# Kernel optimization log

Hardware: AMD Instinct MI355X
Metric: run time of the kernel (lower is better)

## Reference

```python
import jax, jax.numpy as jnp
import numpy as np

N_NODES, N_EDGES, N_LAYERS, N_CH, N_GRAPHS = 50000, 1600000, 4, 16, 64
HID = N_CH * 3  # 16x1o -> dim 48

_eps = np.zeros((3, 3, 3), dtype=np.float32)
_eps[0, 1, 2] = _eps[1, 2, 0] = _eps[2, 0, 1] = 1.0
_eps[0, 2, 1] = _eps[2, 1, 0] = _eps[1, 0, 2] = -1.0
EPS = jnp.asarray(_eps)  # Levi-Civita: CG coeffs for 1 (x) 1 -> 1
TP_NORM = 1.0 / np.sqrt(2.0 * N_CH).astype(np.float32)  # CG norm * path fan-in norm


def setup_inputs():
    key = jax.random.key(0)
    ks = jax.random.split(key, 12)
    return {
        "x": jax.random.normal(ks[0], (N_NODES, 3), jnp.float32),
        "edge_index": jax.random.randint(ks[1], (2, N_EDGES), 0, N_NODES, jnp.int32),
        "edge_attr": jax.random.normal(ks[2], (N_EDGES, 5), jnp.float32),
        "batch": jnp.sort(jax.random.randint(ks[3], (N_NODES,), 0, N_GRAPHS, jnp.int32)),
        "embed_w": jax.random.normal(ks[4], (3, HID), jnp.float32) * 0.3,
        "mlp1_w": jax.random.normal(ks[5], (N_LAYERS, 3, 16), jnp.float32) * 0.5,
        "mlp1_b": jnp.zeros((N_LAYERS, 16), jnp.float32),
        "mlp2_w": jax.random.normal(ks[6], (N_LAYERS, 16, HID), jnp.float32) * 0.25,
        "mlp2_b": jnp.zeros((N_LAYERS, HID), jnp.float32),
        "tp_w": jax.random.normal(ks[7], (N_LAYERS, N_CH, N_CH), jnp.float32),
        "lin_w": jax.random.normal(ks[8], (HID, 1), jnp.float32) * 0.1,
        "lin_b": jnp.zeros((1,), jnp.float32),
    }


def reference(x, edge_index, edge_attr, batch, embed_w, mlp1_w, mlp1_b,
              mlp2_w, mlp2_b, tp_w, lin_w, lin_b):
    n = x.shape[0]
    e = edge_attr.shape[0]
    src, dst = edge_index[0], edge_index[1]

    h = x @ embed_w  # [N, 48] node embedding

    r_ij = edge_attr[:, 2:5]                            # [E, 3]
    r2 = jnp.sum(r_ij * r_ij, axis=-1, keepdims=True)   # [E, 1]
    rhat = r_ij / jnp.maximum(jnp.sqrt(r2), 1e-12)
    sh = jnp.sqrt(3.0) * rhat                            # l=1 SH, component norm
    edge_scalar = jnp.concatenate([edge_attr[:, 0:2], r2], axis=-1)  # [E, 3]

    for l in range(N_LAYERS):
        gate = jax.nn.silu(edge_scalar @ mlp1_w[l] + mlp1_b[l]) @ mlp2_w[l] + mlp2_b[l]  # [E,48]
        xj = h[src].reshape(e, N_CH, 3)                  # gather neighbor feats
        # fully-connected tensor product 16x1o (x) 1o -> 16x1o (cross-product CG)
        tp = jnp.einsum('kij,eui,ej,uv->evk', EPS, xj, sh, tp_w[l]) * TP_NORM
        msg = gate * tp.reshape(e, HID)
        dx = jax.ops.segment_sum(msg, dst, num_segments=n)  # scatter-add
        h = h + dx  # residual

    sums = jax.ops.segment_sum(h, batch, num_segments=N_GRAPHS)
    cnt = jax.ops.segment_sum(jnp.ones((n,), h.dtype), batch, num_segments=N_GRAPHS)
    pooled = sums / jnp.maximum(cnt, 1.0)[:, None]       # global mean pool
    return (pooled @ lin_w + lin_b).ravel()              # [B]
```

## Files before the change

### kernel.cpp

```cpp
#include <hip/hip_runtime.h>

#define N_NODES 50000
#define N_EDGES 1600000
#define N_LAYERS 4
#define N_CH 16
#define HID 48
#define N_GRAPHS 64
#define TP_NORM 0.17677669529663687f
#define SQRT3 1.7320508075688772f
#define REB 256
#define MPAD 28
#define NBLK (N_EDGES / REB)
#define NPART ((N_NODES + 255) / 256)

__device__ __forceinline__ unsigned bfpack2(float a, float b) {
    unsigned ua = __float_as_uint(a);
    unsigned ub = __float_as_uint(b);
    ua = (ua + 0x7fffu + ((ua >> 16) & 1u)) >> 16;
    ub = (ub + 0x7fffu + ((ub >> 16) & 1u)) >> 16;
    return ua | (ub << 16);
}
#define BFLO(u) __uint_as_float((u) << 16)
#define BFHI(u) __uint_as_float((u) & 0xffff0000u)

__global__ void k_embed(const float* __restrict__ x, const float* __restrict__ ew,
                        float* __restrict__ h) {
    int t = blockIdx.x * blockDim.x + threadIdx.x;
    if (t >= N_NODES * HID) return;
    int n = t / HID, c = t % HID;
    h[t] = x[n * 3 + 0] * ew[c] + x[n * 3 + 1] * ew[HID + c] + x[n * 3 + 2] * ew[2 * HID + c];
}

__global__ void k_count(const int* __restrict__ ei, int* __restrict__ cnt,
                        int* __restrict__ rank) {
    int e = blockIdx.x * 256 + threadIdx.x;
    rank[e] = atomicAdd(&cnt[ei[N_EDGES + e]], 1);
}

__global__ void k_sred(const int* __restrict__ cnt, int* __restrict__ bsum) {
    __shared__ int red[256];
    int b = blockIdx.x, t = threadIdx.x;
    int idx = b * 256 + t;
    red[t] = (idx < N_NODES) ? cnt[idx] : 0;
    __syncthreads();
    for (int d = 128; d > 0; d >>= 1) {
        if (t < d) red[t] += red[t + d];
        __syncthreads();
    }
    if (t == 0) bsum[b] = red[0];
}

__global__ void k_sscan(const int* __restrict__ bsum, int* __restrict__ bbase) {
    __shared__ int s[256];
    int t = threadIdx.x;
    int v = (t < NPART) ? bsum[t] : 0;
    s[t] = v;
    __syncthreads();
    for (int d = 1; d < 256; d <<= 1) {
        int x = (t >= d) ? s[t - d] : 0;
        __syncthreads();
        s[t] += x;
        __syncthreads();
    }
    if (t < NPART) bbase[t] = s[t] - v;
    if (t == NPART - 1) bbase[NPART] = s[t];
}

__global__ void k_soff(const int* __restrict__ cnt, const int* __restrict__ bbase,
                       int* __restrict__ off) {
    __shared__ int s[256];
    int b = blockIdx.x, t = threadIdx.x;
    int idx = b * 256 + t;
    int v = (idx < N_NODES) ? cnt[idx] : 0;
    s[t] = v;
    __syncthreads();
    for (int d = 1; d < 256; d <<= 1) {
        int x = (t >= d) ? s[t - d] : 0;
        __syncthreads();
        s[t] += x;
        __syncthreads();
    }
    if (idx < N_NODES) off[idx] = bbase[b] + s[t] - v;
    if (idx == 0) off[N_NODES] = bbase[NPART];
}

__global__ void k_rng(const int* __restrict__ off, int* __restrict__ blk) {
    int b = blockIdx.x * blockDim.x + threadIdx.x;
    if (b >= NBLK) return;
    int base = b * REB;
    int lo = 0, hi = N_NODES;
    while (lo < hi) { int mid = (lo + hi + 1) >> 1; if (off[mid] <= base) lo = mid; else hi = mid - 1; }
    blk[2 * b] = lo;
    int last = base + REB - 1;
    int hi2 = N_NODES;
    while (lo < hi2) { int mid = (lo + hi2 + 1) >> 1; if (off[mid] <= last) lo = mid; else hi2 = mid - 1; }
    blk[2 * b + 1] = lo;
}

__global__ void k_build(const int* __restrict__ ei, const float* __restrict__ ea,
                        const int* __restrict__ off, const int* __restrict__ rank,
                        float* __restrict__ es_s) {
    int e = blockIdx.x * 256 + threadIdx.x;
    int d = ei[N_EDGES + e];
    int pos = off[d] + rank[e];
    float a0 = ea[e * 5 + 0], a1 = ea[e * 5 + 1];
    float rx = ea[e * 5 + 2], ry = ea[e * 5 + 3], rz = ea[e * 5 + 4];
    float r2 = rx * rx + ry * ry + rz * rz;
    float inv = rsqrtf(fmaxf(r2, 1e-24f)) * SQRT3;
    float4* o = (float4*)(es_s + (size_t)pos * 8);
    o[0] = make_float4(a0, a1, r2, rx * inv);
    o[1] = make_float4(ry * inv, rz * inv, __int_as_float(ei[e]), 0.f);
}

__global__ void k_h2(const float* __restrict__ hin, const float* __restrict__ tpw,
                     unsigned* __restrict__ h2, float* __restrict__ dx) {
    int t = blockIdx.x * blockDim.x + threadIdx.x;
    if (t >= N_NODES * 24) return;
    int n = t / 24, p = t % 24;
    int c0 = 2 * p, c1 = c0 + 1;
    int v0 = c0 / 3, i0 = c0 % 3;
    int v1 = c1 / 3, i1 = c1 % 3;
    const float* hr = hin + (size_t)n * HID;
    float s0 = 0.f, s1 = 0.f;
#pragma unroll
    for (int u = 0; u < 16; u++) {
        s0 = fmaf(tpw[u * 16 + v0], hr[u * 3 + i0], s0);
        s1 = fmaf(tpw[u * 16 + v1], hr[u * 3 + i1], s1);
    }
    h2[t] = bfpack2(s0, s1);
    *(float2*)(dx + (size_t)n * HID + c0) = make_float2(0.f, 0.f);
}

__global__ void k_h2_add(const float* __restrict__ hin, const float* __restrict__ dxin,
                         const float* __restrict__ tpw,
                         unsigned* __restrict__ h2, float* __restrict__ hout,
                         float* __restrict__ dxout) {
    int t = blockIdx.x * blockDim.x + threadIdx.x;
    if (t >= N_NODES * 24) return;
    int n = t / 24, p = t % 24;
    int c0 = 2 * p, c1 = c0 + 1;
    int v0 = c0 / 3, i0 = c0 % 3;
    int v1 = c1 / 3, i1 = c1 % 3;
    size_t rb = (size_t)n * HID;
    const float* hr = hin + rb;
    const float* dr = dxin + rb;
    float s0 = 0.f, s1 = 0.f;
#pragma unroll
    for (int u = 0; u < 16; u++) {
        float e0 = hr[u * 3 + i0] + dr[u * 3 + i0];
        float e1 = hr[u * 3 + i1] + dr[u * 3 + i1];
        s0 = fmaf(tpw[u * 16 + v0], e0, s0);
        s1 = fmaf(tpw[u * 16 + v1], e1, s1);
    }
    h2[t] = bfpack2(s0, s1);
    float2 hv = *(const float2*)(hr + c0);
    float2 dv = *(const float2*)(dr + c0);
    *(float2*)(hout + rb + c0) = make_float2(hv.x + dv.x, hv.y + dv.y);
    *(float2*)(dxout + rb + c0) = make_float2(0.f, 0.f);
}

__global__ void __launch_bounds__(256) k_fused(
    const float* __restrict__ es_s, const int* __restrict__ off,
    const int* __restrict__ blk,
    const unsigned* __restrict__ h2, float* __restrict__ dx,
    const float* __restrict__ m1w, const float* __restrict__ m1b,
    const float* __restrict__ m2w, const float* __restrict__ m2b)
{
    __shared__ float s_msg[REB][MPAD];

    int t = threadIdx.x;
    int base = blockIdx.x * REB;
    int e2 = base + t;

    const float4* esp = (const float4*)(es_s + (size_t)e2 * 8);
    float4 es0 = esp[0];
    float4 es1 = esp[1];
    int src = __float_as_int(es1.z);
    const uint4* hv = (const uint4*)(h2 + (size_t)src * 24);
    uint4 A0 = hv[0], A1 = hv[1], A2 = hv[2];
    int n0 = blk[2 * blockIdx.x];
    int n1 = blk[2 * blockIdx.x + 1];

    float a0 = es0.x, a1 = es0.y, r2 = es0.z;
    float shx = es0.w, shy = es1.x, shz = es1.y;

    float hid[16];
#pragma unroll
    for (int j = 0; j < 16; j++) {
        float z = fmaf(a0, m1w[j], fmaf(a1, m1w[16 + j], fmaf(r2, m1w[32 + j], m1b[j])));
        hid[j] = z / (1.f + __expf(-z));
    }

    int gid = t / 12;
    int rem = t % 12;
    int q   = rem >> 1;
    int half= rem & 1;

    float xj[24];
#define UNPK8(u, d) { (d)[0]=BFLO((u).x); (d)[1]=BFHI((u).x); (d)[2]=BFLO((u).y); (d)[3]=BFHI((u).y); \
                      (d)[4]=BFLO((u).z); (d)[5]=BFHI((u).z); (d)[6]=BFLO((u).w); (d)[7]=BFHI((u).w); }
    UNPK8(A0, &xj[0]); UNPK8(A1, &xj[8]); UNPK8(A2, &xj[16]);

    float m[24];
#pragma unroll
    for (int qq = 0; qq < 6; qq++) {
        float4 b = *(const float4*)(m2b + qq * 4);
        m[qq * 4 + 0] = b.x; m[qq * 4 + 1] = b.y; m[qq * 4 + 2] = b.z; m[qq * 4 + 3] = b.w;
    }
#pragma unroll
    for (int j = 0; j < 16; j++) {
        float hj = hid[j];
#pragma unroll
        for (int qq = 0; qq < 6; qq++) {
            float4 w4 = *(const float4*)(m2w + j * 48 + qq * 4);
            m[qq * 4 + 0] = fmaf(hj, w4.x, m[qq * 4 + 0]);
            m[qq * 4 + 1] = fmaf(hj, w4.y, m[qq * 4 + 1]);
            m[qq * 4 + 2] = fmaf(hj, w4.z, m[qq * 4 + 2]);
            m[qq * 4 + 3] = fmaf(hj, w4.w, m[qq * 4 + 3]);
        }
    }
#pragma unroll
    for (int v = 0; v < 8; v++) {
        float x0 = xj[v * 3 + 0], x1 = xj[v * 3 + 1], x2 = xj[v * 3 + 2];
        float c0 = x1 * shz - x2 * shy;
        float c1 = x2 * shx - x0 * shz;
        float c2 = x0 * shy - x1 * shx;
        m[v * 3 + 0] *= c0 * TP_NORM;
        m[v * 3 + 1] *= c1 * TP_NORM;
        m[v * 3 + 2] *= c2 * TP_NORM;
    }
    {
        float4* row = (float4*)&s_msg[t][0];
#pragma unroll
        for (int qq = 0; qq < 6; qq++) row[qq] = ((float4*)m)[qq];
    }
    {
        uint4 B0 = hv[3], B1 = hv[4], B2 = hv[5];
        UNPK8(B0, &xj[0]); UNPK8(B1, &xj[8]); UNPK8(B2, &xj[16]);
    }
    __syncthreads();

    if (t < 252) {
        for (int nn = n0 + gid; nn <= n1; nn += 21) {
            int lo = off[nn], hi = off[nn + 1];
            int rlo = (lo > base) ? lo - base : 0;
            int rhi = ((hi < base + REB) ? hi : base + REB) - base;
            if (rlo < rhi) {
                float4 acc = make_float4(0.f, 0.f, 0.f, 0.f);
                for (int r = rlo + half; r < rhi; r += 2) {
                    float4 v = *(const float4*)&s_msg[r][q * 4];
                    acc.x += v.x; acc.y += v.y; acc.z += v.z; acc.w += v.w;
                }
                acc.x += __shfl_xor(acc.x, 1);
                acc.y += __shfl_xor(acc.y, 1);
                acc.z += __shfl_xor(acc.z, 1);
                acc.w += __shfl_xor(acc.w, 1);
                if (half == 0) {
                    float* dp = dx + (size_t)nn * HID + q * 4;
                    if (lo < base || hi > base + REB) {
                        atomicAdd(dp + 0, acc.x); atomicAdd(dp + 1, acc.y);
                        atomicAdd(dp + 2, acc.z); atomicAdd(dp + 3, acc.w);
                    } else {
                        *(float4*)dp = acc;
                    }
                }
            }
        }
    }
    __syncthreads();

#pragma unroll
    for (int qq = 0; qq < 6; qq++) {
        float4 b = *(const float4*)(m2b + 24 + qq * 4);
        m[qq * 4 + 0] = b.x; m[qq * 4 + 1] = b.y; m[qq * 4 + 2] = b.z; m[qq * 4 + 3] = b.w;
    }
#pragma unroll
    for (int j = 0; j < 16; j++) {
        float hj = hid[j];
#pragma unroll
        for (int qq = 0; qq < 6; qq++) {
            float4 w4 = *(const float4*)(m2w + j * 48 + 24 + qq * 4);
            m[qq * 4 + 0] = fmaf(hj, w4.x, m[qq * 4 + 0]);
            m[qq * 4 + 1] = fmaf(hj, w4.y, m[qq * 4 + 1]);
            m[qq * 4 + 2] = fmaf(hj, w4.z, m[qq * 4 + 2]);
            m[qq * 4 + 3] = fmaf(hj, w4.w, m[qq * 4 + 3]);
        }
    }
#pragma unroll
    for (int v = 0; v < 8; v++) {
        float x0 = xj[v * 3 + 0], x1 = xj[v * 3 + 1], x2 = xj[v * 3 + 2];
        float c0 = x1 * shz - x2 * shy;
        float c1 = x2 * shx - x0 * shz;
        float c2 = x0 * shy - x1 * shx;
        m[v * 3 + 0] *= c0 * TP_NORM;
        m[v * 3 + 1] *= c1 * TP_NORM;
        m[v * 3 + 2] *= c2 * TP_NORM;
    }
    {
        float4* row = (float4*)&s_msg[t][0];
#pragma unroll
        for (int qq = 0; qq < 6; qq++) row[qq] = ((float4*)m)[qq];
    }
    __syncthreads();

    if (t < 252) {
        for (int nn = n0 + gid; nn <= n1; nn += 21) {
            int lo = off[nn], hi = off[nn + 1];
            int rlo = (lo > base) ? lo - base : 0;
            int rhi = ((hi < base + REB) ? hi : base + REB) - base;
            if (rlo < rhi) {
                float4 acc = make_float4(0.f, 0.f, 0.f, 0.f);
                for (int r = rlo + half; r < rhi; r += 2) {
                    float4 v = *(const float4*)&s_msg[r][q * 4];
                    acc.x += v.x; acc.y += v.y; acc.z += v.z; acc.w += v.w;
                }
                acc.x += __shfl_xor(acc.x, 1);
                acc.y += __shfl_xor(acc.y, 1);
                acc.z += __shfl_xor(acc.z, 1);
                acc.w += __shfl_xor(acc.w, 1);
                if (half == 0) {
                    float* dp = dx + (size_t)nn * HID + 24 + q * 4;
                    if (lo < base || hi > base + REB) {
                        atomicAdd(dp + 0, acc.x); atomicAdd(dp + 1, acc.y);
                        atomicAdd(dp + 2, acc.z); atomicAdd(dp + 3, acc.w);
                    } else {
                        *(float4*)dp = acc;
                    }
                }
            }
        }
    }
}

__global__ void k_add(float* __restrict__ h, float* __restrict__ dx) {
    int t = blockIdx.x * blockDim.x + threadIdx.x;
    if (t >= N_NODES * HID) return;
    h[t] += dx[t];
    dx[t] = 0.f;
}

__global__ void __launch_bounds__(256) k_pool(
    const float* __restrict__ h, const float* __restrict__ dxin, const int* __restrict__ batch,
    const float* __restrict__ linw, float* __restrict__ gsum, float* __restrict__ gcnt)
{
    __shared__ float ss[N_GRAPHS];
    __shared__ float sc[N_GRAPHS];
    for (int i = threadIdx.x; i < N_GRAPHS; i += 256) { ss[i] = 0.f; sc[i] = 0.f; }
    __syncthreads();
    int n = blockIdx.x * 256 + threadIdx.x;
    if (n < N_NODES) {
        float s = 0.f;
        const float4* hv = (const float4*)(h + (size_t)n * HID);
        const float4* dv = (const float4*)(dxin + (size_t)n * HID);
#pragma unroll
        for (int qq = 0; qq < 12; qq++) {
            float4 v = hv[qq], d = dv[qq];
            s += (v.x + d.x) * linw[qq * 4 + 0] + (v.y + d.y) * linw[qq * 4 + 1]
               + (v.z + d.z) * linw[qq * 4 + 2] + (v.w + d.w) * linw[qq * 4 + 3];
        }
        int b = batch[n];
        atomicAdd(&ss[b], s);
        atomicAdd(&sc[b], 1.f);
    }
    __syncthreads();
    for (int i = threadIdx.x; i < N_GRAPHS; i += 256) {
        if (sc[i] != 0.f) {
            atomicAdd(&gsum[i], ss[i]);
            atomicAdd(&gcnt[i], sc[i]);
        }
    }
}

__global__ void k_final(const float* __restrict__ gsum, const float* __restrict__ gcnt,
                        const float* __restrict__ linb, float* __restrict__ out) {
    int g = threadIdx.x;
    if (g < N_GRAPHS) out[g] = gsum[g] / fmaxf(gcnt[g], 1.f) + linb[0];
}

__global__ void __launch_bounds__(256) k_edge_atomic(
    const int* __restrict__ ei, const float* __restrict__ ea,
    const float* __restrict__ h, float* __restrict__ dx,
    const float* __restrict__ m1w, const float* __restrict__ m1b,
    const float* __restrict__ m2w, const float* __restrict__ m2b,
    const float* __restrict__ tpw)
{
    __shared__ float s_m1w[48];
    __shared__ float s_m1b[16];
    __shared__ float s_m2w[768];
    __shared__ float s_m2b[48];
    __shared__ float s_tpw[256];
    for (int i = threadIdx.x; i < 48;  i += 256) s_m1w[i] = m1w[i];
    for (int i = threadIdx.x; i < 16;  i += 256) s_m1b[i] = m1b[i];
    for (int i = threadIdx.x; i < 768; i += 256) s_m2w[i] = m2w[i];
    for (int i = threadIdx.x; i < 48;  i += 256) s_m2b[i] = m2b[i];
    for (int i = threadIdx.x; i < 256; i += 256) s_tpw[i] = tpw[i];
    __syncthreads();
    int e = blockIdx.x * 256 + threadIdx.x;
    int src = ei[e];
    int dst = ei[N_EDGES + e];
    float a0 = ea[e * 5 + 0], a1 = ea[e * 5 + 1];
    float rx = ea[e * 5 + 2], ry = ea[e * 5 + 3], rz = ea[e * 5 + 4];
    float r2 = rx * rx + ry * ry + rz * rz;
    float inv = rsqrtf(fmaxf(r2, 1e-24f));
    float shx = SQRT3 * rx * inv, shy = SQRT3 * ry * inv, shz = SQRT3 * rz * inv;
    float hid[16];
#pragma unroll
    for (int j = 0; j < 16; j++) {
        float z = a0 * s_m1w[j] + a1 * s_m1w[16 + j] + r2 * s_m1w[32 + j] + s_m1b[j];
        hid[j] = z / (1.f + __expf(-z));
    }
    float xj[48];
    const float4* hv = (const float4*)(h + (size_t)src * HID);
#pragma unroll
    for (int qq = 0; qq < 12; qq++) {
        float4 v = hv[qq];
        xj[qq * 4 + 0] = v.x; xj[qq * 4 + 1] = v.y; xj[qq * 4 + 2] = v.z; xj[qq * 4 + 3] = v.w;
    }
    float cr[48];
#pragma unroll
    for (int u = 0; u < 16; u++) {
        float x0 = xj[u * 3 + 0], x1 = xj[u * 3 + 1], x2 = xj[u * 3 + 2];
        cr[u * 3 + 0] = x1 * shz - x2 * shy;
        cr[u * 3 + 1] = x2 * shx - x0 * shz;
        cr[u * 3 + 2] = x0 * shy - x1 * shx;
    }
    float* dd = dx + (size_t)dst * HID;
#pragma unroll
    for (int v = 0; v < 16; v++) {
        float t0 = 0.f, t1 = 0.f, t2 = 0.f;
#pragma unroll
        for (int u = 0; u < 16; u++) {
            float w = s_tpw[u * 16 + v];
            t0 += w * cr[u * 3 + 0];
            t1 += w * cr[u * 3 + 1];
            t2 += w * cr[u * 3 + 2];
        }
        float g0 = s_m2b[v * 3 + 0], g1 = s_m2b[v * 3 + 1], g2 = s_m2b[v * 3 + 2];
#pragma unroll
        for (int j = 0; j < 16; j++) {
            float hj = hid[j];
            g0 = fmaf(hj, s_m2w[j * 48 + v * 3 + 0], g0);
            g1 = fmaf(hj, s_m2w[j * 48 + v * 3 + 1], g1);
            g2 = fmaf(hj, s_m2w[j * 48 + v * 3 + 2], g2);
        }
        atomicAdd(dd + v * 3 + 0, g0 * t0 * TP_NORM);
        atomicAdd(dd + v * 3 + 1, g1 * t1 * TP_NORM);
        atomicAdd(dd + v * 3 + 2, g2 * t2 * TP_NORM);
    }
}

extern "C" void kernel_launch(void* const* d_in, const int* in_sizes, int n_in,
                              void* d_out, int out_size, void* d_ws, size_t ws_size,
                              hipStream_t stream) {
    const float* x    = (const float*)d_in[0];
    const int*   ei   = (const int*)  d_in[1];
    const float* ea   = (const float*)d_in[2];
    const int*   batch= (const int*)  d_in[3];
    const float* ew   = (const float*)d_in[4];
    const float* m1w  = (const float*)d_in[5];
    const float* m1b  = (const float*)d_in[6];
    const float* m2w  = (const float*)d_in[7];
    const float* m2b  = (const float*)d_in[8];
    const float* tpw  = (const float*)d_in[9];
    const float* linw = (const float*)d_in[10];
    const float* linb = (const float*)d_in[11];
    float* out = (float*)d_out;

    char* w = (char*)d_ws;
    auto alloc = [&](size_t bytes) -> char* {
        char* p = w;
        w += (bytes + 255) & ~(size_t)255;
        return p;
    };
    float*    hA   = (float*)   alloc((size_t)N_NODES * HID * 4);
    float*    hB   = (float*)   alloc((size_t)N_NODES * HID * 4);
    unsigned* h2   = (unsigned*)alloc((size_t)N_NODES * 24 * 4);
    float*    dxA  = (float*)   alloc((size_t)N_NODES * HID * 4);
    float*    dxB  = (float*)   alloc((size_t)N_NODES * HID * 4);
    float*    gbuf = (float*)   alloc(2 * N_GRAPHS * 4);
    float*    es_s = (float*)   alloc((size_t)N_EDGES * 8 * 4);
    int*      off  = (int*)     alloc((size_t)(N_NODES + 1) * 4);
    int*      cnt  = (int*)     alloc((size_t)N_NODES * 4);
    int*      rank = (int*)     alloc((size_t)N_EDGES * 4);
    int*      blk  = (int*)     alloc((size_t)NBLK * 2 * 4);
    int*      bsum = (int*)     alloc((size_t)NPART * 4);
    int*      bbase= (int*)     alloc((size_t)(NPART + 1) * 4);
    size_t need = (size_t)(w - (char*)d_ws);
    float* gsum = gbuf;
    float* gcnt = gbuf + N_GRAPHS;

    if (ws_size < need) {
        float* fh   = (float*)d_ws;
        float* fdx  = fh + (size_t)N_NODES * HID;
        float* fgs  = fdx + (size_t)N_NODES * HID;
        float* fgc  = fgs + N_GRAPHS;
        hipMemsetAsync(fdx, 0, ((size_t)N_NODES * HID + 2 * N_GRAPHS) * sizeof(float), stream);
        k_embed<<<(N_NODES * HID + 255) / 256, 256, 0, stream>>>(x, ew, fh);
        for (int l = 0; l < N_LAYERS; l++) {
            k_edge_atomic<<<N_EDGES / 256, 256, 0, stream>>>(ei, ea, fh, fdx,
                m1w + l * 48, m1b + l * 16, m2w + l * 768, m2b + l * 48, tpw + l * 256);
            k_add<<<(N_NODES * HID + 255) / 256, 256, 0, stream>>>(fh, fdx);
        }
        hipMemsetAsync(fdx, 0, (size_t)N_NODES * HID * 4, stream);
        k_pool<<<(N_NODES + 255) / 256, 256, 0, stream>>>(fh, fdx, batch, linw, fgs, fgc);
        k_final<<<1, 64, 0, stream>>>(fgs, fgc, linb, out);
        return;
    }

    hipMemsetAsync(cnt, 0, (size_t)N_NODES * 4, stream);
    hipMemsetAsync(gbuf, 0, 2 * N_GRAPHS * 4, stream);
    k_count<<<N_EDGES / 256, 256, 0, stream>>>(ei, cnt, rank);
    k_sred<<<NPART, 256, 0, stream>>>(cnt, bsum);
    k_sscan<<<1, 256, 0, stream>>>(bsum, bbase);
    k_soff<<<NPART, 256, 0, stream>>>(cnt, bbase, off);
    k_rng<<<(NBLK + 255) / 256, 256, 0, stream>>>(off, blk);
    k_build<<<N_EDGES / 256, 256, 0, stream>>>(ei, ea, off, rank, es_s);

    k_embed<<<(N_NODES * HID + 255) / 256, 256, 0, stream>>>(x, ew, hA);

    const int npBlocks = (N_NODES * 24 + 255) / 256;
    float* dxs[2] = { dxA, dxB };
    float* hcur = hA;
    float* hnxt = hB;
    for (int l = 0; l < N_LAYERS; l++) {
        float* dxw = dxs[l & 1];
        if (l == 0) {
            k_h2<<<npBlocks, 256, 0, stream>>>(hcur, tpw, h2, dxw);
        } else {
            k_h2_add<<<npBlocks, 256, 0, stream>>>(hcur, dxs[(l - 1) & 1], tpw + l * 256,
                                                   h2, hnxt, dxw);
            float* tmp = hcur; hcur = hnxt; hnxt = tmp;
        }
        k_fused<<<NBLK, 256, 0, stream>>>(es_s, off, blk, h2, dxw,
            m1w + l * 48, m1b + l * 16, m2w + l * 768, m2b + l * 48);
    }

    k_pool<<<(N_NODES + 255) / 256, 256, 0, stream>>>(hcur, dxs[(N_LAYERS - 1) & 1],
                                                      batch, linw, gsum, gcnt);
    k_final<<<1, 64, 0, stream>>>(gsum, gcnt, linb, out);
}
```

Before: 466.6 us.

## Pack sorted edge records into 16-byte bf16 format and use packed FMA for gate MLP

Edge records (edge scalars, spherical harmonics, src index) are compressed from 32 bytes to 16 bytes by storing the float fields as bf16 pairs, halving the per-edge stream read in every layer. The gate MLP's second matmul is rewritten with 2-wide float vectors and elementwise fma so the compiler can emit packed FMA instructions. The trade-off is reduced precision of the edge attributes, r2 and spherical harmonics, which may affect accuracy.

```diff
diff --git a/kernel.cpp b/kernel.cpp
--- a/kernel.cpp
+++ b/kernel.cpp
@@ -13,6 +13,8 @@
 #define NBLK (N_EDGES / REB)
 #define NPART ((N_NODES + 255) / 256)
 
+typedef float v2f __attribute__((ext_vector_type(2)));
+
 __device__ __forceinline__ unsigned bfpack2(float a, float b) {
     unsigned ua = __float_as_uint(a);
     unsigned ub = __float_as_uint(b);
@@ -99,7 +101,7 @@
 
 __global__ void k_build(const int* __restrict__ ei, const float* __restrict__ ea,
                         const int* __restrict__ off, const int* __restrict__ rank,
-                        float* __restrict__ es_s) {
+                        uint4* __restrict__ es_s) {
     int e = blockIdx.x * 256 + threadIdx.x;
     int d = ei[N_EDGES + e];
     int pos = off[d] + rank[e];
@@ -107,9 +109,12 @@
     float rx = ea[e * 5 + 2], ry = ea[e * 5 + 3], rz = ea[e * 5 + 4];
     float r2 = rx * rx + ry * ry + rz * rz;
     float inv = rsqrtf(fmaxf(r2, 1e-24f)) * SQRT3;
-    float4* o = (float4*)(es_s + (size_t)pos * 8);
-    o[0] = make_float4(a0, a1, r2, rx * inv);
-    o[1] = make_float4(ry * inv, rz * inv, __int_as_float(ei[e]), 0.f);
+    uint4 o;
+    o.x = bfpack2(a0, a1);
+    o.y = bfpack2(r2, rx * inv);
+    o.z = bfpack2(ry * inv, rz * inv);
+    o.w = (unsigned)ei[e];
+    es_s[pos] = o;
 }
 
 __global__ void k_h2(const float* __restrict__ hin, const float* __restrict__ tpw,
@@ -160,7 +165,7 @@
 }
 
 __global__ void __launch_bounds__(256) k_fused(
-    const float* __restrict__ es_s, const int* __restrict__ off,
+    const uint4* __restrict__ es_s, const int* __restrict__ off,
     const int* __restrict__ blk,
     const unsigned* __restrict__ h2, float* __restrict__ dx,
     const float* __restrict__ m1w, const float* __restrict__ m1b,
@@ -172,17 +177,16 @@
     int base = blockIdx.x * REB;
     int e2 = base + t;
 
-    const float4* esp = (const float4*)(es_s + (size_t)e2 * 8);
-    float4 es0 = esp[0];
-    float4 es1 = esp[1];
-    int src = __float_as_int(es1.z);
+    uint4 rec = es_s[e2];
+    int src = (int)rec.w;
     const uint4* hv = (const uint4*)(h2 + (size_t)src * 24);
     uint4 A0 = hv[0], A1 = hv[1], A2 = hv[2];
     int n0 = blk[2 * blockIdx.x];
     int n1 = blk[2 * blockIdx.x + 1];
 
-    float a0 = es0.x, a1 = es0.y, r2 = es0.z;
-    float shx = es0.w, shy = es1.x, shz = es1.y;
+    float a0 = BFLO(rec.x), a1 = BFHI(rec.x);
+    float r2 = BFLO(rec.y), shx = BFHI(rec.y);
+    float shy = BFLO(rec.z), shz = BFHI(rec.z);
 
     float hid[16];
 #pragma unroll
@@ -201,22 +205,23 @@
                       (d)[4]=BFLO((u).z); (d)[5]=BFHI((u).z); (d)[6]=BFLO((u).w); (d)[7]=BFHI((u).w); }
     UNPK8(A0, &xj[0]); UNPK8(A1, &xj[8]); UNPK8(A2, &xj[16]);
 
-    float m[24];
+    alignas(16) v2f mv[12];
+    float* m = (float*)mv;
+
 #pragma unroll
     for (int qq = 0; qq < 6; qq++) {
         float4 b = *(const float4*)(m2b + qq * 4);
-        m[qq * 4 + 0] = b.x; m[qq * 4 + 1] = b.y; m[qq * 4 + 2] = b.z; m[qq * 4 + 3] = b.w;
+        mv[2 * qq + 0] = (v2f){b.x, b.y};
+        mv[2 * qq + 1] = (v2f){b.z, b.w};
     }
 #pragma unroll
     for (int j = 0; j < 16; j++) {
-        float hj = hid[j];
+        v2f hj2 = (v2f){hid[j], hid[j]};
 #pragma unroll
         for (int qq = 0; qq < 6; qq++) {
             float4 w4 = *(const float4*)(m2w + j * 48 + qq * 4);
-            m[qq * 4 + 0] = fmaf(hj, w4.x, m[qq * 4 + 0]);
-            m[qq * 4 + 1] = fmaf(hj, w4.y, m[qq * 4 + 1]);
-            m[qq * 4 + 2] = fmaf(hj, w4.z, m[qq * 4 + 2]);
-            m[qq * 4 + 3] = fmaf(hj, w4.w, m[qq * 4 + 3]);
+            mv[2 * qq + 0] = __builtin_elementwise_fma(hj2, (v2f){w4.x, w4.y}, mv[2 * qq + 0]);
+            mv[2 * qq + 1] = __builtin_elementwise_fma(hj2, (v2f){w4.z, w4.w}, mv[2 * qq + 1]);
         }
     }
 #pragma unroll
@@ -272,18 +277,17 @@
 #pragma unroll
     for (int qq = 0; qq < 6; qq++) {
         float4 b = *(const float4*)(m2b + 24 + qq * 4);
-        m[qq * 4 + 0] = b.x; m[qq * 4 + 1] = b.y; m[qq * 4 + 2] = b.z; m[qq * 4 + 3] = b.w;
+        mv[2 * qq + 0] = (v2f){b.x, b.y};
+        mv[2 * qq + 1] = (v2f){b.z, b.w};
     }
 #pragma unroll
     for (int j = 0; j < 16; j++) {
-        float hj = hid[j];
+        v2f hj2 = (v2f){hid[j], hid[j]};
 #pragma unroll
         for (int qq = 0; qq < 6; qq++) {
             float4 w4 = *(const float4*)(m2w + j * 48 + 24 + qq * 4);
-            m[qq * 4 + 0] = fmaf(hj, w4.x, m[qq * 4 + 0]);
-            m[qq * 4 + 1] = fmaf(hj, w4.y, m[qq * 4 + 1]);
-            m[qq * 4 + 2] = fmaf(hj, w4.z, m[qq * 4 + 2]);
-            m[qq * 4 + 3] = fmaf(hj, w4.w, m[qq * 4 + 3]);
+            mv[2 * qq + 0] = __builtin_elementwise_fma(hj2, (v2f){w4.x, w4.y}, mv[2 * qq + 0]);
+            mv[2 * qq + 1] = __builtin_elementwise_fma(hj2, (v2f){w4.z, w4.w}, mv[2 * qq + 1]);
         }
     }
 #pragma unroll
@@ -478,7 +482,7 @@
     float*    dxA  = (float*)   alloc((size_t)N_NODES * HID * 4);
     float*    dxB  = (float*)   alloc((size_t)N_NODES * HID * 4);
     float*    gbuf = (float*)   alloc(2 * N_GRAPHS * 4);
-    float*    es_s = (float*)   alloc((size_t)N_EDGES * 8 * 4);
+    uint4*    es_s = (uint4*)   alloc((size_t)N_EDGES * 16);
     int*      off  = (int*)     alloc((size_t)(N_NODES + 1) * 4);
     int*      cnt  = (int*)     alloc((size_t)N_NODES * 4);
     int*      rank = (int*)     alloc((size_t)N_EDGES * 4);
```

Measured after the change: 450.1 us. 3.5% less time.
